# Optimization experiments

Hardware: AMD Instinct MI355X
Metric: run time of the kernel (lower is better)

Reference implementation:

```python
import jax, jax.numpy as jnp
import numpy as np

ATT_DIM = 512
HEADS = 8
HEAD_DIM = ATT_DIM // HEADS
D_IN = 512
LEFT_MASK = 256
RIGHT_MASK = 0
LARGE = 1e30


def pos_encoding(S, d):
    # Transformer-XL sinusoid table over relative positions S-1 .. -(S-1), length 2S-1.
    inv_freq = (1.0 / (10000.0 ** (np.arange(0, d, 2.0) / d))).astype(np.float32)
    pos = jnp.arange(S - 1, -S, -1, dtype=jnp.float32)          # [2S-1]
    ang = pos[:, None] * jnp.asarray(inv_freq)[None, :]          # [2S-1, d/2]
    # concat([sin, cos], -1) on a trailing singleton -> interleaved sin/cos per frequency
    return jnp.stack([jnp.sin(ang), jnp.cos(ang)], axis=-1).reshape(2 * S - 1, d)


def rel_shift(x):
    # x: [B, N, S, 2S-1] -> [B, N, S, S] with out[i, j] = x[i, S-1 - i + j]
    B, N, S, L = x.shape
    x = jnp.pad(x, ((0, 0), (0, 0), (0, 0), (1, 0)))             # [B,N,S,L+1]
    x = x.reshape(B, N, L + 1, S)[:, :, 1:, :]                   # [B,N,L,S]
    x = x.reshape(B, N, S, L)
    return x[:, :, :, :S]


def setup_inputs() -> dict:
    key = jax.random.key(0)
    ks = jax.random.split(key, 9)
    B, S, D = 2, 2048, D_IN
    scale = 0.02
    return {
        "x": jax.random.normal(ks[0], (B, S, D), dtype=jnp.float32),
        "Wq": jax.random.normal(ks[1], (D, ATT_DIM), dtype=jnp.float32) * scale,
        "b_con": jax.random.normal(ks[2], (ATT_DIM,), dtype=jnp.float32) * scale,
        "b_rel": jax.random.normal(ks[3], (ATT_DIM,), dtype=jnp.float32) * scale,
        "Wk": jax.random.normal(ks[4], (D, ATT_DIM), dtype=jnp.float32) * scale,
        "Wkr": jax.random.normal(ks[5], (D_IN, ATT_DIM), dtype=jnp.float32) * scale,
        "Wv": jax.random.normal(ks[6], (D, ATT_DIM), dtype=jnp.float32) * scale,
        "bv": jax.random.normal(ks[7], (ATT_DIM,), dtype=jnp.float32) * scale,
        "x_len": jax.random.randint(ks[8], (B,), 1, S + 1).astype(jnp.int32),
    }


def reference(x, Wq, b_con, b_rel, Wk, Wkr, Wv, bv, x_len):
    B, S, D = x.shape
    N, Dh = HEADS, HEAD_DIM

    # content/relative query share the kernel (TiedDense) with separate biases
    q_lin = jnp.einsum('bsd,de->bse', x, Wq)
    q_con = (q_lin + b_con).reshape(B, S, N, Dh)
    q_rel = (q_lin + b_rel).reshape(B, S, N, Dh)
    k_con = jnp.einsum('bsd,de->bse', x, Wk).reshape(B, S, N, Dh)

    content_energy = jnp.einsum('bind,bjnd->bnij', q_con, k_con)  # [B,N,S,S]

    pos_emb = pos_encoding(S, D_IN)                               # [2S-1, D]
    k_rel = (pos_emb @ Wkr).reshape(2 * S - 1, N, Dh)
    relative_energy = jnp.einsum('bind,jnd->bnij', q_rel, k_rel)  # [B,N,S,2S-1]
    relative_energy = rel_shift(relative_energy)                  # [B,N,S,S]

    energy = (content_energy + relative_energy) / jnp.sqrt(jnp.float32(Dh))

    # sequence mask over keys (broadcast [B,1,1,S]) * banded mask (band_part)
    j = jnp.arange(S)
    seq_mask = (j[None, :] < x_len[:, None]).astype(jnp.float32)[:, None, None, :]
    i = jnp.arange(S)[:, None]
    band = ((i - j[None, :] <= LEFT_MASK) & (j[None, :] - i <= RIGHT_MASK)).astype(jnp.float32)
    mask = seq_mask * band[None, None, :, :]

    masked_energy = energy - (1.0 - mask) * LARGE
    attention = jax.nn.softmax(masked_energy, axis=-1)

    v = (jnp.einsum('bsd,de->bse', x, Wv) + bv).reshape(B, S, N, Dh)
    context = jnp.einsum('bnij,bjnd->bind', attention, v).reshape(B, S, N * Dh)
    return context
```

## Files before the change

kernel.cpp:

```cpp
#include <hip/hip_runtime.h>
#include <math.h>

#define S_ 2048
#define NH 8
#define CSL 320
#define LP 72

typedef __attribute__((ext_vector_type(8))) short short8;
typedef __attribute__((ext_vector_type(4))) float f32x4;
typedef unsigned short ushort_t;

__device__ __forceinline__ short bf16r(float x) {
    union { float f; unsigned u; } v; v.f = x;
    unsigned r = v.u + 0x7fffu + ((v.u >> 16) & 1u);
    return (short)(r >> 16);
}
__device__ __forceinline__ float b2f(ushort_t h) {
    union { float f; unsigned u; } v; v.u = ((unsigned)h) << 16; return v.f;
}

__global__ __launch_bounds__(256) void prep_kernel(
    const float* __restrict__ x,
    const float* __restrict__ Wq, const float* __restrict__ Wk,
    const float* __restrict__ Wv, const float* __restrict__ Wkr,
    ushort_t* __restrict__ WTq, ushort_t* __restrict__ WTk,
    ushort_t* __restrict__ WTv, ushort_t* __restrict__ WTkr,
    ushort_t* __restrict__ pos, ushort_t* __restrict__ xb16)
{
    const int widx = blockIdx.z;
    const int t = threadIdx.x;
    if (widx == 4) {
        const int base = blockIdx.y * 8 + blockIdx.x;
        const float C = -0.051905126482615036f;
        const int f = t;
#pragma unroll
        for (int rep = 0; rep < 6; ++rep) {
            const int r = base + rep * 64;
            unsigned pk = 0;
            if (r <= 256) {
                float ang = (float)r * exp2f(C * (float)f);
                unsigned s = (unsigned)(ushort_t)bf16r(sinf(ang));
                unsigned c = (unsigned)(ushort_t)bf16r(cosf(ang));
                pk = s | (c << 16);
            }
            ((unsigned*)pos)[(size_t)r * 256 + f] = pk;
        }
        return;
    }
    if (widx == 5) {
        const int sub = blockIdx.y * 8 + blockIdx.x;
        const size_t base = (size_t)sub * 32768;
#pragma unroll
        for (int it = 0; it < 8; ++it) {
            const size_t idx = base + (size_t)it * 4096 + (size_t)t * 16;
            const float* src = &x[idx];
            ushort_t t16[16];
#pragma unroll
            for (int u = 0; u < 16; ++u) t16[u] = (ushort_t)bf16r(src[u]);
            *(short8*)&xb16[idx]     = *(short8*)&t16[0];
            *(short8*)&xb16[idx + 8] = *(short8*)&t16[8];
        }
        return;
    }
    const float* W = (widx == 0) ? Wq : (widx == 1) ? Wk : (widx == 2) ? Wv : Wkr;
    ushort_t* WT   = (widx == 0) ? WTq : (widx == 1) ? WTk : (widx == 2) ? WTv : WTkr;
    const int k0 = blockIdx.x * 64, n0 = blockIdx.y * 64;
    __shared__ __align__(16) ushort_t T[64][72];
    const int srow = t >> 2, sc0 = (t & 3) * 16;
    const float* src = &W[(size_t)(k0 + srow) * 512 + n0 + sc0];
#pragma unroll
    for (int u = 0; u < 16; ++u) T[sc0 + u][srow] = (ushort_t)bf16r(src[u]);
    __syncthreads();
    ushort_t* dst = &WT[(size_t)(n0 + srow) * 512 + k0 + sc0];
    *(short8*)dst       = *(const short8*)&T[srow][sc0];
    *(short8*)(dst + 8) = *(const short8*)&T[srow][sc0 + 8];
}

__global__ __launch_bounds__(256) void qkv_gemm(
    const ushort_t* __restrict__ xb16,
    const ushort_t* __restrict__ WTq, const ushort_t* __restrict__ WTk,
    const ushort_t* __restrict__ WTv,
    const ushort_t* __restrict__ pos, const ushort_t* __restrict__ WTkr,
    const float* __restrict__ b_con, const float* __restrict__ b_rel,
    const float* __restrict__ bv, const int* __restrict__ xlen_p,
    ushort_t* __restrict__ qcon, ushort_t* __restrict__ qrel,
    ushort_t* __restrict__ kout, ushort_t* __restrict__ vT,
    ushort_t* __restrict__ krel)
{
    const int widx = blockIdx.y >> 3;
    const int tid = threadIdx.x, lane = tid & 63, w = tid >> 6;
    const int quad = lane >> 4, l16 = lane & 15;

    __shared__ __align__(16) ushort_t A_lds[128][40];
    __shared__ __align__(16) ushort_t B_lds[64][40];

    f32x4 acc[2][4];
#pragma unroll
    for (int mt = 0; mt < 2; ++mt)
#pragma unroll
        for (int nt = 0; nt < 4; ++nt) acc[mt][nt] = (f32x4){0.f, 0.f, 0.f, 0.f};

    const int arow = tid >> 1, ak0 = (tid & 1) * 16;
    const int brow = tid >> 2, bk0 = (tid & 3) * 8;

    if (widx < 2) {
        const int m0 = blockIdx.x * 128;
        {
            const int xl = xlen_p[m0 >> 11];
            const int s0 = m0 & 2047;
            if (widx == 0) { if (s0 >= xl + 256) return; }
            else           { if (s0 >= xl + 63)  return; }
        }
        const int n0 = (blockIdx.y & 7) * 64;
        const ushort_t* WT = (widx == 0) ? WTq : WTk;
        const ushort_t* xrow = &xb16[(size_t)(m0 + arow) * 512 + ak0];
        const ushort_t* wrow = &WT[(size_t)(n0 + brow) * 512 + bk0];

        short8 pa0 = *(const short8*)xrow;
        short8 pa1 = *(const short8*)(xrow + 8);
        short8 pb  = *(const short8*)wrow;

#pragma unroll 1
        for (int k0 = 0; k0 < 512; k0 += 32) {
            __syncthreads();
            *(short8*)&A_lds[arow][ak0]     = pa0;
            *(short8*)&A_lds[arow][ak0 + 8] = pa1;
            *(short8*)&B_lds[brow][bk0]     = pb;
            if (k0 < 480) {
                pa0 = *(const short8*)(xrow + k0 + 32);
                pa1 = *(const short8*)(xrow + k0 + 40);
                pb  = *(const short8*)(wrow + k0 + 32);
            }
            __syncthreads();
            short8 a0 = *(const short8*)&A_lds[w * 32 + l16][quad * 8];
            short8 a1 = *(const short8*)&A_lds[w * 32 + 16 + l16][quad * 8];
#pragma unroll
            for (int nt = 0; nt < 4; ++nt) {
                short8 bb = *(const short8*)&B_lds[nt * 16 + l16][quad * 8];
                acc[0][nt] = __builtin_amdgcn_mfma_f32_16x16x32_bf16(a0, bb, acc[0][nt], 0, 0, 0);
                acc[1][nt] = __builtin_amdgcn_mfma_f32_16x16x32_bf16(a1, bb, acc[1][nt], 0, 0, 0);
            }
        }

#pragma unroll
        for (int nt = 0; nt < 4; ++nt) {
            const int col = n0 + nt * 16 + l16;
            float bc = 0.f, br = 0.f;
            if (widx == 0) { bc = b_con[col]; br = b_rel[col]; }
#pragma unroll
            for (int mt = 0; mt < 2; ++mt) {
#pragma unroll
                for (int reg = 0; reg < 4; ++reg) {
                    const size_t m = (size_t)(m0 + w * 32 + mt * 16 + quad * 4 + reg);
                    const float val = acc[mt][nt][reg];
                    if (widx == 0) {
                        qcon[m * 512 + col] = (ushort_t)bf16r((val + bc) * 0.125f);
                        qrel[m * 512 + col] = (ushort_t)bf16r((val + br) * 0.125f);
                    } else {
                        kout[m * 512 + col] = (ushort_t)bf16r(val);
                    }
                }
            }
        }
    } else if (widx == 2) {
        const int vb = (blockIdx.y & 7) * 32 + blockIdx.x;
        const int m0d = (vb & 3) * 128;
        const int n0j = (vb >> 2) * 64;
        const ushort_t* wrow = &WTv[(size_t)(m0d + arow) * 512 + ak0];
        const ushort_t* xrow = &xb16[(size_t)(n0j + brow) * 512 + bk0];

        short8 pa0 = *(const short8*)wrow;
        short8 pa1 = *(const short8*)(wrow + 8);
        short8 pb  = *(const short8*)xrow;

#pragma unroll 1
        for (int k0 = 0; k0 < 512; k0 += 32) {
            __syncthreads();
            *(short8*)&A_lds[arow][ak0]     = pa0;
            *(short8*)&A_lds[arow][ak0 + 8] = pa1;
            *(short8*)&B_lds[brow][bk0]     = pb;
            if (k0 < 480) {
                pa0 = *(const short8*)(wrow + k0 + 32);
                pa1 = *(const short8*)(wrow + k0 + 40);
                pb  = *(const short8*)(xrow + k0 + 32);
            }
            __syncthreads();
            short8 a0 = *(const short8*)&A_lds[w * 32 + l16][quad * 8];
            short8 a1 = *(const short8*)&A_lds[w * 32 + 16 + l16][quad * 8];
#pragma unroll
            for (int nt = 0; nt < 4; ++nt) {
                short8 bb = *(const short8*)&B_lds[nt * 16 + l16][quad * 8];
                acc[0][nt] = __builtin_amdgcn_mfma_f32_16x16x32_bf16(a0, bb, acc[0][nt], 0, 0, 0);
                acc[1][nt] = __builtin_amdgcn_mfma_f32_16x16x32_bf16(a1, bb, acc[1][nt], 0, 0, 0);
            }
        }

        const int b = n0j >> 11;
#pragma unroll
        for (int mt = 0; mt < 2; ++mt) {
#pragma unroll
            for (int reg = 0; reg < 4; ++reg) {
                const int d = m0d + w * 32 + mt * 16 + quad * 4 + reg;
                const int n = d >> 6, dd = d & 63;
                const float bvv = bv[d];
#pragma unroll
                for (int nt = 0; nt < 4; ++nt) {
                    const int s = (n0j + nt * 16 + l16) & 2047;
                    vT[((size_t)((b * NH + n) * 64 + dd)) * 2048 + s] =
                        (ushort_t)bf16r(acc[mt][nt][reg] + bvv);
                }
            }
        }
    } else {
        if (blockIdx.x >= 24) return;
        const int m0 = (blockIdx.x >> 3) * 128;
        const int n0 = (blockIdx.x & 7) * 64;
        const ushort_t* prow = &pos[(size_t)(m0 + arow) * 512 + ak0];
        const ushort_t* wrow = &WTkr[(size_t)(n0 + brow) * 512 + bk0];

        short8 pa0 = *(const short8*)prow;
        short8 pa1 = *(const short8*)(prow + 8);
        short8 pb  = *(const short8*)wrow;

#pragma unroll 1
        for (int k0 = 0; k0 < 512; k0 += 32) {
            __syncthreads();
            *(short8*)&A_lds[arow][ak0]     = pa0;
            *(short8*)&A_lds[arow][ak0 + 8] = pa1;
            *(short8*)&B_lds[brow][bk0]     = pb;
            if (k0 < 480) {
                pa0 = *(const short8*)(prow + k0 + 32);
                pa1 = *(const short8*)(prow + k0 + 40);
                pb  = *(const short8*)(wrow + k0 + 32);
            }
            __syncthreads();
            short8 a0 = *(const short8*)&A_lds[w * 32 + l16][quad * 8];
            short8 a1 = *(const short8*)&A_lds[w * 32 + 16 + l16][quad * 8];
#pragma unroll
            for (int nt = 0; nt < 4; ++nt) {
                short8 bb = *(const short8*)&B_lds[nt * 16 + l16][quad * 8];
                acc[0][nt] = __builtin_amdgcn_mfma_f32_16x16x32_bf16(a0, bb, acc[0][nt], 0, 0, 0);
                acc[1][nt] = __builtin_amdgcn_mfma_f32_16x16x32_bf16(a1, bb, acc[1][nt], 0, 0, 0);
            }
        }

#pragma unroll
        for (int nt = 0; nt < 4; ++nt) {
            const int col = n0 + nt * 16 + l16;
#pragma unroll
            for (int mt = 0; mt < 2; ++mt)
#pragma unroll
                for (int reg = 0; reg < 4; ++reg) {
                    const size_t m = (size_t)(m0 + w * 32 + mt * 16 + quad * 4 + reg);
                    krel[m * 512 + col] = (ushort_t)bf16r(acc[mt][nt][reg]);
                }
        }
    }
}

__global__ __launch_bounds__(256) void rel_gemm(
    const ushort_t* __restrict__ qrel, const ushort_t* __restrict__ krel,
    const ushort_t* __restrict__ vT, const int* __restrict__ xlen_p,
    ushort_t* __restrict__ R3, float* __restrict__ vmean)
{
    const int tile = blockIdx.x, n = blockIdx.y, b = blockIdx.z;
    const int tid = threadIdx.x, lane = tid & 63, w = tid >> 6;
    const int quad = lane >> 4, l16 = lane & 15;

    __shared__ __align__(16) ushort_t A_lds[128][LP];
    __shared__ __align__(16) ushort_t B_lds[64][LP];

    if (tile == 16) {
        const int row = tid >> 2, seg = tid & 3;
        const ushort_t* src = &vT[((size_t)((b * NH + n) * 64 + row)) * 2048 + seg * 512];
        float sum = 0.f;
        for (int it = 0; it < 64; ++it) {
            short8 h = *(const short8*)(src + it * 8);
#pragma unroll
            for (int u = 0; u < 8; ++u) sum += b2f((ushort_t)h[u]);
        }
        float* scratch = (float*)A_lds;
        scratch[row * 4 + seg] = sum;
        __syncthreads();
        if (tid < 64) {
            float s = scratch[tid * 4] + scratch[tid * 4 + 1]
                    + scratch[tid * 4 + 2] + scratch[tid * 4 + 3];
            vmean[(size_t)b * 512 + n * 64 + tid] = s * (1.0f / (float)S_);
        }
        return;
    }

    const int i0 = tile * 128;
    if (i0 >= xlen_p[b] + 256) return;

    {
        const int srow = tid >> 1, sc0 = (tid & 1) * 32;
        const ushort_t* src = &qrel[((size_t)b * S_ + i0 + srow) * 512 + n * 64 + sc0];
#pragma unroll
        for (int u = 0; u < 4; ++u)
            *(short8*)&A_lds[srow][sc0 + u * 8] = *(const short8*)(src + u * 8);
    }

    const size_t rbase3 = (size_t)(b * NH + n) * S_ * CSL;
    const int srow2 = tid >> 2, sc2 = (tid & 3) * 16;

    short8 pb0, pb1;
    auto issueB = [&](int rc) {
        const ushort_t* src = &krel[(size_t)(rc * 64 + srow2) * 512 + n * 64 + sc2];
        pb0 = *(const short8*)src;
        pb1 = *(const short8*)(src + 8);
    };
    issueB(0);

#pragma unroll 1
    for (int rc = 0; rc < 5; ++rc) {
        __syncthreads();
        *(short8*)&B_lds[srow2][sc2]     = pb0;
        *(short8*)&B_lds[srow2][sc2 + 8] = pb1;
        if (rc < 4) issueB(rc + 1);
        __syncthreads();

        short8 a[2][2];
#pragma unroll
        for (int mt = 0; mt < 2; ++mt) {
            a[mt][0] = *(const short8*)&A_lds[w * 32 + mt * 16 + l16][quad * 8];
            a[mt][1] = *(const short8*)&A_lds[w * 32 + mt * 16 + l16][quad * 8 + 32];
        }
#pragma unroll
        for (int nt = 0; nt < 4; ++nt) {
            short8 b0 = *(const short8*)&B_lds[nt * 16 + l16][quad * 8];
            short8 b1 = *(const short8*)&B_lds[nt * 16 + l16][quad * 8 + 32];
            const int r = rc * 64 + nt * 16 + l16;
#pragma unroll
            for (int mt = 0; mt < 2; ++mt) {
                f32x4 s = (f32x4){0.f, 0.f, 0.f, 0.f};
                s = __builtin_amdgcn_mfma_f32_16x16x32_bf16(a[mt][0], b0, s, 0, 0, 0);
                s = __builtin_amdgcn_mfma_f32_16x16x32_bf16(a[mt][1], b1, s, 0, 0, 0);
                if (r <= 256) {
#pragma unroll
                    for (int reg = 0; reg < 4; ++reg) {
                        const int ig = i0 + w * 32 + mt * 16 + quad * 4 + reg;
                        const int cslot = (ig & 63) + 256 - r;
                        R3[rbase3 + (size_t)ig * CSL + cslot] = (ushort_t)bf16r(s[reg]);
                    }
                }
            }
        }
    }
}

__global__ __launch_bounds__(256) void attn_kernel(
    const ushort_t* __restrict__ qcon, const ushort_t* __restrict__ kbuf,
    const ushort_t* __restrict__ vT, const ushort_t* __restrict__ R3,
    const float* __restrict__ vmean, const int* __restrict__ xlen_p,
    float* __restrict__ out)
{
    const int bx = blockIdx.x;
    const int tile = ((bx & 7) << 2) | (bx >> 3);
    const int n = blockIdx.y, b = blockIdx.z;
    const int i0 = tile * 64;
    const int tid = threadIdx.x, lane = tid & 63, w = tid >> 6;
    const int quad = lane >> 4, l16 = lane & 15;
    const int xlen = xlen_p[b];

    if (i0 >= xlen + 256) {
        const int row = tid >> 2, cf = (tid & 3) * 16;
        const float* vm = &vmean[(size_t)b * 512 + n * 64 + cf];
        float* dst = &out[((size_t)b * S_ + i0 + row) * 512 + n * 64 + cf];
#pragma unroll
        for (int u = 0; u < 16; u += 4)
            *(float4*)&dst[u] = *(const float4*)&vm[u];
        return;
    }
    int nchunk = (xlen - i0 + 256 + 63) >> 6;
    if (nchunk > 5) nchunk = 5;
    const int c0 = (i0 < 256) ? ((256 - i0) >> 6) : 0;

    __shared__ __align__(16) ushort_t k_lds[64][LP];
    __shared__ __align__(16) ushort_t vT_lds[64][LP];
    __shared__ __align__(16) ushort_t Rl_lds[64][LP];

    const ushort_t* qc = &qcon[((size_t)b * S_ + i0 + w * 16 + l16) * 512 + n * 64 + quad * 8];
    const short8 aq0 = *(const short8*)qc;
    const short8 aq1 = *(const short8*)(qc + 32);

    f32x4 Oa[4];
#pragma unroll
    for (int nt = 0; nt < 4; ++nt) Oa[nt] = (f32x4){0.f, 0.f, 0.f, 0.f};
    float lpart[4] = {};

    const size_t rbase3 = (size_t)(b * NH + n) * S_ * CSL;
    const size_t vTbase = (size_t)((b * NH + n) * 64) * 2048;
    const int srow = tid >> 2, sc0 = (tid & 3) * 16;

    short8 kr[2], vr[2], rr[2], kn[2], vn[2], rn[2];

    auto issue = [&](int c, short8* kd, short8* vd, short8* rd) {
        const int jc0 = i0 - 256 + c * 64;
        const ushort_t* ks = &kbuf[((size_t)b * S_ + jc0 + srow) * 512 + n * 64 + sc0];
        kd[0] = *(const short8*)ks;
        kd[1] = *(const short8*)(ks + 8);
        const ushort_t* vs = &vT[vTbase + (size_t)srow * 2048 + jc0 + sc0];
        vd[0] = *(const short8*)vs;
        vd[1] = *(const short8*)(vs + 8);
        const ushort_t* Rs = &R3[rbase3 + (size_t)(i0 + srow) * CSL + c * 64 + sc0];
        rd[0] = *(const short8*)Rs;
        rd[1] = *(const short8*)(Rs + 8);
    };

    issue(c0, kr, vr, rr);

#pragma unroll 1
    for (int c = c0; c < nchunk; ++c) {
        const int jc0 = i0 - 256 + c * 64;
        __syncthreads();
        *(short8*)&k_lds[srow][sc0]      = kr[0];
        *(short8*)&k_lds[srow][sc0 + 8]  = kr[1];
        *(short8*)&vT_lds[srow][sc0]     = vr[0];
        *(short8*)&vT_lds[srow][sc0 + 8] = vr[1];
        *(short8*)&Rl_lds[srow][sc0]     = rr[0];
        *(short8*)&Rl_lds[srow][sc0 + 8] = rr[1];
        if (c + 1 < nchunk) issue(c + 1, kn, vn, rn);
        __syncthreads();

        f32x4 Sacc[4];
#pragma unroll
        for (int jt = 0; jt < 4; ++jt) {
            short8 bk0 = *(const short8*)&k_lds[jt * 16 + l16][quad * 8];
            short8 bk1 = *(const short8*)&k_lds[jt * 16 + l16][quad * 8 + 32];
            f32x4 s = (f32x4){0.f, 0.f, 0.f, 0.f};
            s = __builtin_amdgcn_mfma_f32_16x16x32_bf16(aq0, bk0, s, 0, 0, 0);
            s = __builtin_amdgcn_mfma_f32_16x16x32_bf16(aq1, bk1, s, 0, 0, 0);
            Sacc[jt] = s;
        }

#pragma unroll
        for (int jt = 0; jt < 4; ++jt) {
#pragma unroll
            for (int reg = 0; reg < 4; ++reg) {
                const int row = w * 16 + quad * 4 + reg;
                const int i = i0 + row;
                const int j = jc0 + jt * 16 + l16;
                const int r = i - j;
                const bool valid = (j < xlen) && (r >= 0) && (r <= 256);
                float rvv = b2f(Rl_lds[row][jt * 16 + l16]);
                float e = valid ? __expf(Sacc[jt][reg] + rvv) : 0.f;
                lpart[reg] += e;
                Rl_lds[row][jt * 16 + l16] = (ushort_t)bf16r(e);
            }
        }

        short8 ap0 = *(const short8*)&Rl_lds[w * 16 + l16][quad * 8];
        short8 ap1 = *(const short8*)&Rl_lds[w * 16 + l16][quad * 8 + 32];
#pragma unroll
        for (int nt = 0; nt < 4; ++nt) {
            short8 bv0 = *(const short8*)&vT_lds[nt * 16 + l16][quad * 8];
            short8 bv1 = *(const short8*)&vT_lds[nt * 16 + l16][quad * 8 + 32];
            Oa[nt] = __builtin_amdgcn_mfma_f32_16x16x32_bf16(ap0, bv0, Oa[nt], 0, 0, 0);
            Oa[nt] = __builtin_amdgcn_mfma_f32_16x16x32_bf16(ap1, bv1, Oa[nt], 0, 0, 0);
        }

        kr[0] = kn[0]; kr[1] = kn[1];
        vr[0] = vn[0]; vr[1] = vn[1];
        rr[0] = rn[0]; rr[1] = rn[1];
    }

#pragma unroll
    for (int reg = 0; reg < 4; ++reg) {
#pragma unroll
        for (int off = 1; off < 16; off <<= 1)
            lpart[reg] += __shfl_xor(lpart[reg], off, 64);
    }

#pragma unroll
    for (int reg = 0; reg < 4; ++reg) {
        const int i = i0 + w * 16 + quad * 4 + reg;
        const bool dead = (i >= xlen + 256);
        const float linv = 1.0f / lpart[reg];
#pragma unroll
        for (int nt = 0; nt < 4; ++nt) {
            const int d = n * 64 + nt * 16 + l16;
            float val = dead ? vmean[(size_t)b * 512 + d] : Oa[nt][reg] * linv;
            out[((size_t)b * S_ + i) * 512 + d] = val;
        }
    }
}

extern "C" void kernel_launch(void* const* d_in, const int* in_sizes, int n_in,
                              void* d_out, int out_size, void* d_ws, size_t ws_size,
                              hipStream_t stream) {
    const float* x     = (const float*)d_in[0];
    const float* Wq    = (const float*)d_in[1];
    const float* b_con = (const float*)d_in[2];
    const float* b_rel = (const float*)d_in[3];
    const float* Wk    = (const float*)d_in[4];
    const float* Wkr   = (const float*)d_in[5];
    const float* Wv    = (const float*)d_in[6];
    const float* bv    = (const float*)d_in[7];
    const int*   xlen  = (const int*)d_in[8];
    float* out = (float*)d_out;

    float* ws = (float*)d_ws;
    float* vmean = ws;
    ushort_t* ub   = (ushort_t*)(vmean + 1024);
    ushort_t* R3   = ub;
    ushort_t* qcon = R3   + 10485760;
    ushort_t* kbuf = qcon + 2097152;
    ushort_t* vT   = kbuf + 2097152;
    ushort_t* qrel = vT   + 2097152;
    ushort_t* xb16 = qrel + 2097152;
    ushort_t* krel = xb16 + 2097152;
    ushort_t* pos  = krel + 196608;
    ushort_t* WTq  = pos  + 196608;
    ushort_t* WTk  = WTq + 262144;
    ushort_t* WTv  = WTk + 262144;
    ushort_t* WTkr = WTv + 262144;

    prep_kernel<<<dim3(8, 8, 6), 256, 0, stream>>>(x, Wq, Wk, Wv, Wkr,
                                                   WTq, WTk, WTv, WTkr, pos, xb16);
    qkv_gemm<<<dim3(32, 25), 256, 0, stream>>>(xb16, WTq, WTk, WTv, pos, WTkr,
                                               b_con, b_rel, bv, xlen,
                                               qcon, qrel, kbuf, vT, krel);
    rel_gemm<<<dim3(17, 8, 2), 256, 0, stream>>>(qrel, krel, vT, xlen, R3, vmean);
    attn_kernel<<<dim3(32, 8, 2), 256, 0, stream>>>(qcon, kbuf, vT, R3, vmean,
                                                    xlen, out);
}
```

Before: 127.4 us.

## Fuse rel-energy GEMM into Q projection and compute krel and vmean in prep

Drops the separate rel_gemm launch. The Q-projection blocks now keep q_rel in LDS and immediately compute the banded relative-energy tile into R3, so q_rel no longer goes through global memory. The k_rel projection moves into prep_kernel, which generates the sinusoid table on the fly and transposes Wkr inline, replacing the separate pos and WTkr buffers. vmean is now derived from mean(x) @ Wv + bv using column partial sums computed in prep, rather than by summing vT. This saves a launch and several global round trips, but makes the Q blocks longer and puts sin/cos evaluation on the krel GEMM path.

After: 152.1 us. 1.19x slower.

```diff
diff --git a/kernel.cpp b/kernel.cpp
--- a/kernel.cpp
+++ b/kernel.cpp
@@ -24,30 +24,17 @@
     const float* __restrict__ Wq, const float* __restrict__ Wk,
     const float* __restrict__ Wv, const float* __restrict__ Wkr,
     ushort_t* __restrict__ WTq, ushort_t* __restrict__ WTk,
-    ushort_t* __restrict__ WTv, ushort_t* __restrict__ WTkr,
-    ushort_t* __restrict__ pos, ushort_t* __restrict__ xb16)
+    ushort_t* __restrict__ WTv, ushort_t* __restrict__ xb16,
+    float* __restrict__ xpart, ushort_t* __restrict__ krel)
 {
     const int widx = blockIdx.z;
     const int t = threadIdx.x;
-    if (widx == 4) {
-        const int base = blockIdx.y * 8 + blockIdx.x;
-        const float C = -0.051905126482615036f;
-        const int f = t;
-#pragma unroll
-        for (int rep = 0; rep < 6; ++rep) {
-            const int r = base + rep * 64;
-            unsigned pk = 0;
-            if (r <= 256) {
-                float ang = (float)r * exp2f(C * (float)f);
-                unsigned s = (unsigned)(ushort_t)bf16r(sinf(ang));
-                unsigned c = (unsigned)(ushort_t)bf16r(cosf(ang));
-                pk = s | (c << 16);
-            }
-            ((unsigned*)pos)[(size_t)r * 256 + f] = pk;
-        }
-        return;
-    }
-    if (widx == 5) {
+
+    __shared__ __align__(16) ushort_t T[64][72];
+    __shared__ __align__(16) ushort_t Ak[128][40];
+    __shared__ __align__(16) ushort_t Bk[64][40];
+
+    if (widx == 3) {
         const int sub = blockIdx.y * 8 + blockIdx.x;
         const size_t base = (size_t)sub * 32768;
 #pragma unroll
@@ -62,10 +49,90 @@
         }
         return;
     }
-    const float* W = (widx == 0) ? Wq : (widx == 1) ? Wk : (widx == 2) ? Wv : Wkr;
-    ushort_t* WT   = (widx == 0) ? WTq : (widx == 1) ? WTk : (widx == 2) ? WTv : WTkr;
+    if (widx == 4) {
+        const int sub = blockIdx.y * 8 + blockIdx.x;
+        const int b = sub >> 5, rb = sub & 31;
+        const float* src = &x[((size_t)b * 2048 + (size_t)rb * 64) * 512];
+        float s0 = 0.f, s1 = 0.f;
+        for (int r = 0; r < 64; ++r) {
+            s0 += src[(size_t)r * 512 + t];
+            s1 += src[(size_t)r * 512 + t + 256];
+        }
+        xpart[(size_t)sub * 512 + t]       = s0;
+        xpart[(size_t)sub * 512 + t + 256] = s1;
+        return;
+    }
+    if (widx == 5) {
+        const int idx = blockIdx.y * 8 + blockIdx.x;
+        if (idx >= 24) return;
+        const int m0 = (idx >> 3) * 128;
+        const int n0 = (idx & 7) * 64;
+        const int lane = t & 63, w = t >> 6;
+        const int quad = lane >> 4, l16 = lane & 15;
+        const float C = -0.051905126482615036f;
+
+        f32x4 acc[2][4];
+#pragma unroll
+        for (int mt = 0; mt < 2; ++mt)
+#pragma unroll
+            for (int nt = 0; nt < 4; ++nt) acc[mt][nt] = (f32x4){0.f, 0.f, 0.f, 0.f};
+
+        const int arow = t >> 1, af0 = (t & 1) * 16;
+        const int bkr = t >> 3, bc0 = (t & 7) * 8;
+        const int r = m0 + arow;
+
+#pragma unroll 1
+        for (int k0 = 0; k0 < 512; k0 += 32) {
+            __syncthreads();
+            {
+                ushort_t a16[16];
+                if (r <= 256) {
+#pragma unroll
+                    for (int p = 0; p < 8; ++p) {
+                        const int k = k0 + af0 + 2 * p;
+                        const float ang = (float)r * exp2f(C * (float)(k >> 1));
+                        a16[2 * p]     = (ushort_t)bf16r(sinf(ang));
+                        a16[2 * p + 1] = (ushort_t)bf16r(cosf(ang));
+                    }
+                } else {
+#pragma unroll
+                    for (int u = 0; u < 16; ++u) a16[u] = 0;
+                }
+                *(short8*)&Ak[arow][af0]     = *(short8*)&a16[0];
+                *(short8*)&Ak[arow][af0 + 8] = *(short8*)&a16[8];
+            }
+            {
+                const float* wsrc = &Wkr[(size_t)(k0 + bkr) * 512 + n0 + bc0];
+#pragma unroll
+                for (int u = 0; u < 8; ++u)
+                    Bk[bc0 + u][bkr] = (ushort_t)bf16r(wsrc[u]);
+            }
+            __syncthreads();
+            short8 a0 = *(const short8*)&Ak[w * 32 + l16][quad * 8];
+            short8 a1 = *(const short8*)&Ak[w * 32 + 16 + l16][quad * 8];
+#pragma unroll
+            for (int nt = 0; nt < 4; ++nt) {
+                short8 bb = *(const short8*)&Bk[nt * 16 + l16][quad * 8];
+                acc[0][nt] = __builtin_amdgcn_mfma_f32_16x16x32_bf16(a0, bb, acc[0][nt], 0, 0, 0);
+                acc[1][nt] = __builtin_amdgcn_mfma_f32_16x16x32_bf16(a1, bb, acc[1][nt], 0, 0, 0);
+            }
+        }
+#pragma unroll
+        for (int nt = 0; nt < 4; ++nt) {
+            const int col = n0 + nt * 16 + l16;
+#pragma unroll
+            for (int mt = 0; mt < 2; ++mt)
+#pragma unroll
+                for (int reg = 0; reg < 4; ++reg) {
+                    const size_t m = (size_t)(m0 + w * 32 + mt * 16 + quad * 4 + reg);
+                    krel[m * 512 + col] = (ushort_t)bf16r(acc[mt][nt][reg]);
+                }
+        }
+        return;
+    }
+    const float* W = (widx == 0) ? Wq : (widx == 1) ? Wk : Wv;
+    ushort_t* WT   = (widx == 0) ? WTq : (widx == 1) ? WTk : WTv;
     const int k0 = blockIdx.x * 64, n0 = blockIdx.y * 64;
-    __shared__ __align__(16) ushort_t T[64][72];
     const int srow = t >> 2, sc0 = (t & 3) * 16;
     const float* src = &W[(size_t)(k0 + srow) * 512 + n0 + sc0];
 #pragma unroll
@@ -79,20 +146,23 @@
 __global__ __launch_bounds__(256) void qkv_gemm(
     const ushort_t* __restrict__ xb16,
     const ushort_t* __restrict__ WTq, const ushort_t* __restrict__ WTk,
-    const ushort_t* __restrict__ WTv,
-    const ushort_t* __restrict__ pos, const ushort_t* __restrict__ WTkr,
+    const ushort_t* __restrict__ WTv, const ushort_t* __restrict__ krel,
     const float* __restrict__ b_con, const float* __restrict__ b_rel,
     const float* __restrict__ bv, const int* __restrict__ xlen_p,
-    ushort_t* __restrict__ qcon, ushort_t* __restrict__ qrel,
-    ushort_t* __restrict__ kout, ushort_t* __restrict__ vT,
-    ushort_t* __restrict__ krel)
+    const float* __restrict__ xpart,
+    ushort_t* __restrict__ qcon, ushort_t* __restrict__ kout,
+    ushort_t* __restrict__ vT, ushort_t* __restrict__ R3,
+    float* __restrict__ vmean)
 {
     const int widx = blockIdx.y >> 3;
     const int tid = threadIdx.x, lane = tid & 63, w = tid >> 6;
     const int quad = lane >> 4, l16 = lane & 15;
 
-    __shared__ __align__(16) ushort_t A_lds[128][40];
-    __shared__ __align__(16) ushort_t B_lds[64][40];
+    __shared__ __align__(16) ushort_t arena[13824];
+#define AQ(r, c) arena[(r) * 40 + (c)]
+#define BQ(r, c) arena[5120 + (r) * 40 + (c)]
+#define QL(r, c) arena[(r) * 72 + (c)]
+#define BR(r, c) arena[9216 + (r) * 72 + (c)]
 
     f32x4 acc[2][4];
 #pragma unroll
@@ -105,12 +175,10 @@
 
     if (widx < 2) {
         const int m0 = blockIdx.x * 128;
-        {
-            const int xl = xlen_p[m0 >> 11];
-            const int s0 = m0 & 2047;
-            if (widx == 0) { if (s0 >= xl + 256) return; }
-            else           { if (s0 >= xl + 63)  return; }
-        }
+        const int xl = xlen_p[m0 >> 11];
+        const int s0 = m0 & 2047;
+        if (widx == 0) { if (s0 >= xl + 256) return; }
+        else           { if (s0 >= xl + 63)  return; }
         const int n0 = (blockIdx.y & 7) * 64;
         const ushort_t* WT = (widx == 0) ? WTq : WTk;
         const ushort_t* xrow = &xb16[(size_t)(m0 + arow) * 512 + ak0];
@@ -123,41 +191,101 @@
 #pragma unroll 1
         for (int k0 = 0; k0 < 512; k0 += 32) {
             __syncthreads();
-            *(short8*)&A_lds[arow][ak0]     = pa0;
-            *(short8*)&A_lds[arow][ak0 + 8] = pa1;
-            *(short8*)&B_lds[brow][bk0]     = pb;
+            *(short8*)&AQ(arow, ak0)     = pa0;
+            *(short8*)&AQ(arow, ak0 + 8) = pa1;
+            *(short8*)&BQ(brow, bk0)     = pb;
             if (k0 < 480) {
                 pa0 = *(const short8*)(xrow + k0 + 32);
                 pa1 = *(const short8*)(xrow + k0 + 40);
                 pb  = *(const short8*)(wrow + k0 + 32);
             }
             __syncthreads();
-            short8 a0 = *(const short8*)&A_lds[w * 32 + l16][quad * 8];
-            short8 a1 = *(const short8*)&A_lds[w * 32 + 16 + l16][quad * 8];
+            short8 a0 = *(const short8*)&AQ(w * 32 + l16, quad * 8);
+            short8 a1 = *(const short8*)&AQ(w * 32 + 16 + l16, quad * 8);
 #pragma unroll
             for (int nt = 0; nt < 4; ++nt) {
-                short8 bb = *(const short8*)&B_lds[nt * 16 + l16][quad * 8];
+                short8 bb = *(const short8*)&BQ(nt * 16 + l16, quad * 8);
                 acc[0][nt] = __builtin_amdgcn_mfma_f32_16x16x32_bf16(a0, bb, acc[0][nt], 0, 0, 0);
                 acc[1][nt] = __builtin_amdgcn_mfma_f32_16x16x32_bf16(a1, bb, acc[1][nt], 0, 0, 0);
             }
         }
 
+        if (widx == 1) {
+#pragma unroll
+            for (int nt = 0; nt < 4; ++nt) {
+                const int col = n0 + nt * 16 + l16;
+#pragma unroll
+                for (int mt = 0; mt < 2; ++mt)
+#pragma unroll
+                    for (int reg = 0; reg < 4; ++reg) {
+                        const size_t m = (size_t)(m0 + w * 32 + mt * 16 + quad * 4 + reg);
+                        kout[m * 512 + col] = (ushort_t)bf16r(acc[mt][nt][reg]);
+                    }
+            }
+            return;
+        }
+
+        __syncthreads();
 #pragma unroll
         for (int nt = 0; nt < 4; ++nt) {
             const int col = n0 + nt * 16 + l16;
-            float bc = 0.f, br = 0.f;
-            if (widx == 0) { bc = b_con[col]; br = b_rel[col]; }
+            const float bc = b_con[col], br = b_rel[col];
 #pragma unroll
             for (int mt = 0; mt < 2; ++mt) {
 #pragma unroll
                 for (int reg = 0; reg < 4; ++reg) {
-                    const size_t m = (size_t)(m0 + w * 32 + mt * 16 + quad * 4 + reg);
+                    const int rloc = w * 32 + mt * 16 + quad * 4 + reg;
+                    const size_t m = (size_t)(m0 + rloc);
                     const float val = acc[mt][nt][reg];
-                    if (widx == 0) {
-                        qcon[m * 512 + col] = (ushort_t)bf16r((val + bc) * 0.125f);
-                        qrel[m * 512 + col] = (ushort_t)bf16r((val + br) * 0.125f);
-                    } else {
-                        kout[m * 512 + col] = (ushort_t)bf16r(val);
+                    qcon[m * 512 + col] = (ushort_t)bf16r((val + bc) * 0.125f);
+                    QL(rloc, nt * 16 + l16) = (ushort_t)bf16r((val + br) * 0.125f);
+                }
+            }
+        }
+
+        const int b = m0 >> 11, n = n0 >> 6, iloc0 = m0 & 2047;
+        const size_t rbase3 = (size_t)(b * NH + n) * S_ * CSL;
+        const int srow2 = tid >> 2, sc2 = (tid & 3) * 16;
+
+        short8 pb0, pb1;
+        auto issueB = [&](int rc) {
+            const ushort_t* src = &krel[(size_t)(rc * 64 + srow2) * 512 + n0 + sc2];
+            pb0 = *(const short8*)src;
+            pb1 = *(const short8*)(src + 8);
+        };
+        issueB(0);
+
+#pragma unroll 1
+        for (int rc = 0; rc < 5; ++rc) {
+            __syncthreads();
+            *(short8*)&BR(srow2, sc2)     = pb0;
+            *(short8*)&BR(srow2, sc2 + 8) = pb1;
+            if (rc < 4) issueB(rc + 1);
+            __syncthreads();
+
+            short8 a[2][2];
+#pragma unroll
+            for (int mt = 0; mt < 2; ++mt) {
+                a[mt][0] = *(const short8*)&QL(w * 32 + mt * 16 + l16, quad * 8);
+                a[mt][1] = *(const short8*)&QL(w * 32 + mt * 16 + l16, quad * 8 + 32);
+            }
+#pragma unroll
+            for (int nt = 0; nt < 4; ++nt) {
+                short8 b0 = *(const short8*)&BR(nt * 16 + l16, quad * 8);
+                short8 b1 = *(const short8*)&BR(nt * 16 + l16, quad * 8 + 32);
+                const int r = rc * 64 + nt * 16 + l16;
+#pragma unroll
+                for (int mt = 0; mt < 2; ++mt) {
+                    f32x4 s = (f32x4){0.f, 0.f, 0.f, 0.f};
+                    s = __builtin_amdgcn_mfma_f32_16x16x32_bf16(a[mt][0], b0, s, 0, 0, 0);
+                    s = __builtin_amdgcn_mfma_f32_16x16x32_bf16(a[mt][1], b1, s, 0, 0, 0);
+                    if (r <= 256) {
+#pragma unroll
+                        for (int reg = 0; reg < 4; ++reg) {
+                            const int ig = iloc0 + w * 32 + mt * 16 + quad * 4 + reg;
+                            const int cslot = (ig & 63) + 256 - r;
+                            R3[rbase3 + (size_t)ig * CSL + cslot] = (ushort_t)bf16r(s[reg]);
+                        }
                     }
                 }
             }
@@ -176,20 +304,20 @@
 #pragma unroll 1
         for (int k0 = 0; k0 < 512; k0 += 32) {
             __syncthreads();
-            *(short8*)&A_lds[arow][ak0]     = pa0;
-            *(short8*)&A_lds[arow][ak0 + 8] = pa1;
-            *(short8*)&B_lds[brow][bk0]     = pb;
+            *(short8*)&AQ(arow, ak0)     = pa0;
+            *(short8*)&AQ(arow, ak0 + 8) = pa1;
+            *(short8*)&BQ(brow, bk0)     = pb;
             if (k0 < 480) {
                 pa0 = *(const short8*)(wrow + k0 + 32);
                 pa1 = *(const short8*)(wrow + k0 + 40);
                 pb  = *(const short8*)(xrow + k0 + 32);
             }
             __syncthreads();
-            short8 a0 = *(const short8*)&A_lds[w * 32 + l16][quad * 8];
-            short8 a1 = *(const short8*)&A_lds[w * 32 + 16 + l16][quad * 8];
+            short8 a0 = *(const short8*)&AQ(w * 32 + l16, quad * 8);
+            short8 a1 = *(const short8*)&AQ(w * 32 + 16 + l16, quad * 8);
 #pragma unroll
             for (int nt = 0; nt < 4; ++nt) {
-                short8 bb = *(const short8*)&B_lds[nt * 16 + l16][quad * 8];
+                short8 bb = *(const short8*)&BQ(nt * 16 + l16, quad * 8);
                 acc[0][nt] = __builtin_amdgcn_mfma_f32_16x16x32_bf16(a0, bb, acc[0][nt], 0, 0, 0);
                 acc[1][nt] = __builtin_amdgcn_mfma_f32_16x16x32_bf16(a1, bb, acc[1][nt], 0, 0, 0);
             }
@@ -212,141 +340,38 @@
             }
         }
     } else {
-        if (blockIdx.x >= 24) return;
-        const int m0 = (blockIdx.x >> 3) * 128;
-        const int n0 = (blockIdx.x & 7) * 64;
-        const ushort_t* prow = &pos[(size_t)(m0 + arow) * 512 + ak0];
-        const ushort_t* wrow = &WTkr[(size_t)(n0 + brow) * 512 + bk0];
-
-        short8 pa0 = *(const short8*)prow;
-        short8 pa1 = *(const short8*)(prow + 8);
-        short8 pb  = *(const short8*)wrow;
-
-#pragma unroll 1
-        for (int k0 = 0; k0 < 512; k0 += 32) {
-            __syncthreads();
-            *(short8*)&A_lds[arow][ak0]     = pa0;
-            *(short8*)&A_lds[arow][ak0 + 8] = pa1;
-            *(short8*)&B_lds[brow][bk0]     = pb;
-            if (k0 < 480) {
-                pa0 = *(const short8*)(prow + k0 + 32);
-                pa1 = *(const short8*)(prow + k0 + 40);
-                pb  = *(const short8*)(wrow + k0 + 32);
-            }
-            __syncthreads();
-            short8 a0 = *(const short8*)&A_lds[w * 32 + l16][quad * 8];
-            short8 a1 = *(const short8*)&A_lds[w * 32 + 16 + l16][quad * 8];
-#pragma unroll
-            for (int nt = 0; nt < 4; ++nt) {
-                short8 bb = *(const short8*)&B_lds[nt * 16 + l16][quad * 8];
-                acc[0][nt] = __builtin_amdgcn_mfma_f32_16x16x32_bf16(a0, bb, acc[0][nt], 0, 0, 0);
-                acc[1][nt] = __builtin_amdgcn_mfma_f32_16x16x32_bf16(a1, bb, acc[1][nt], 0, 0, 0);
-            }
-        }
-
-#pragma unroll
-        for (int nt = 0; nt < 4; ++nt) {
-            const int col = n0 + nt * 16 + l16;
-#pragma unroll
-            for (int mt = 0; mt < 2; ++mt)
-#pragma unroll
-                for (int reg = 0; reg < 4; ++reg) {
-                    const size_t m = (size_t)(m0 + w * 32 + mt * 16 + quad * 4 + reg);
-                    krel[m * 512 + col] = (ushort_t)bf16r(acc[mt][nt][reg]);
-                }
-        }
-    }
-}
-
-__global__ __launch_bounds__(256) void rel_gemm(
-    const ushort_t* __restrict__ qrel, const ushort_t* __restrict__ krel,
-    const ushort_t* __restrict__ vT, const int* __restrict__ xlen_p,
-    ushort_t* __restrict__ R3, float* __restrict__ vmean)
-{
-    const int tile = blockIdx.x, n = blockIdx.y, b = blockIdx.z;
-    const int tid = threadIdx.x, lane = tid & 63, w = tid >> 6;
-    const int quad = lane >> 4, l16 = lane & 15;
-
-    __shared__ __align__(16) ushort_t A_lds[128][LP];
-    __shared__ __align__(16) ushort_t B_lds[64][LP];
-
-    if (tile == 16) {
-        const int row = tid >> 2, seg = tid & 3;
-        const ushort_t* src = &vT[((size_t)((b * NH + n) * 64 + row)) * 2048 + seg * 512];
-        float sum = 0.f;
-        for (int it = 0; it < 64; ++it) {
-            short8 h = *(const short8*)(src + it * 8);
-#pragma unroll
-            for (int u = 0; u < 8; ++u) sum += b2f((ushort_t)h[u]);
-        }
-        float* scratch = (float*)A_lds;
-        scratch[row * 4 + seg] = sum;
+        if (blockIdx.x >= 8) return;
+        float* xm = (float*)arena;
+        for (int idx = tid; idx < 1024; idx += 256) {
+            const int bb = idx >> 9, k = idx & 511;
+            float s = 0.f;
+            for (int p = 0; p < 32; ++p)
+                s += xpart[(size_t)(bb * 32 + p) * 512 + k];
+            xm[bb * 512 + k] = s * (1.0f / 2048.0f);
+        }
         __syncthreads();
         if (tid < 64) {
-            float s = scratch[tid * 4] + scratch[tid * 4 + 1]
-                    + scratch[tid * 4 + 2] + scratch[tid * 4 + 3];
-            vmean[(size_t)b * 512 + n * 64 + tid] = s * (1.0f / (float)S_);
-        }
-        return;
-    }
-
-    const int i0 = tile * 128;
-    if (i0 >= xlen_p[b] + 256) return;
-
-    {
-        const int srow = tid >> 1, sc0 = (tid & 1) * 32;
-        const ushort_t* src = &qrel[((size_t)b * S_ + i0 + srow) * 512 + n * 64 + sc0];
-#pragma unroll
-        for (int u = 0; u < 4; ++u)
-            *(short8*)&A_lds[srow][sc0 + u * 8] = *(const short8*)(src + u * 8);
-    }
-
-    const size_t rbase3 = (size_t)(b * NH + n) * S_ * CSL;
-    const int srow2 = tid >> 2, sc2 = (tid & 3) * 16;
-
-    short8 pb0, pb1;
-    auto issueB = [&](int rc) {
-        const ushort_t* src = &krel[(size_t)(rc * 64 + srow2) * 512 + n * 64 + sc2];
-        pb0 = *(const short8*)src;
-        pb1 = *(const short8*)(src + 8);
-    };
-    issueB(0);
-
-#pragma unroll 1
-    for (int rc = 0; rc < 5; ++rc) {
-        __syncthreads();
-        *(short8*)&B_lds[srow2][sc2]     = pb0;
-        *(short8*)&B_lds[srow2][sc2 + 8] = pb1;
-        if (rc < 4) issueB(rc + 1);
-        __syncthreads();
-
-        short8 a[2][2];
-#pragma unroll
-        for (int mt = 0; mt < 2; ++mt) {
-            a[mt][0] = *(const short8*)&A_lds[w * 32 + mt * 16 + l16][quad * 8];
-            a[mt][1] = *(const short8*)&A_lds[w * 32 + mt * 16 + l16][quad * 8 + 32];
-        }
-#pragma unroll
-        for (int nt = 0; nt < 4; ++nt) {
-            short8 b0 = *(const short8*)&B_lds[nt * 16 + l16][quad * 8];
-            short8 b1 = *(const short8*)&B_lds[nt * 16 + l16][quad * 8 + 32];
-            const int r = rc * 64 + nt * 16 + l16;
-#pragma unroll
-            for (int mt = 0; mt < 2; ++mt) {
-                f32x4 s = (f32x4){0.f, 0.f, 0.f, 0.f};
-                s = __builtin_amdgcn_mfma_f32_16x16x32_bf16(a[mt][0], b0, s, 0, 0, 0);
-                s = __builtin_amdgcn_mfma_f32_16x16x32_bf16(a[mt][1], b1, s, 0, 0, 0);
-                if (r <= 256) {
-#pragma unroll
-                    for (int reg = 0; reg < 4; ++reg) {
-                        const int ig = i0 + w * 32 + mt * 16 + quad * 4 + reg;
-                        const int cslot = (ig & 63) + 256 - r;
-                        R3[rbase3 + (size_t)ig * CSL + cslot] = (ushort_t)bf16r(s[reg]);
-                    }
+            const int d = blockIdx.x * 64 + tid;
+            const ushort_t* wrow = &WTv[(size_t)d * 512];
+            float a0 = 0.f, a1 = 0.f;
+            for (int k = 0; k < 512; k += 8) {
+                short8 wv = *(const short8*)(wrow + k);
+#pragma unroll
+                for (int u = 0; u < 8; ++u) {
+                    const float wf = b2f((ushort_t)wv[u]);
+                    a0 += xm[k + u] * wf;
+                    a1 += xm[512 + k + u] * wf;
                 }
             }
-        }
-    }
+            const float bvd = bv[d];
+            vmean[d]       = a0 + bvd;
+            vmean[512 + d] = a1 + bvd;
+        }
+    }
+#undef AQ
+#undef BQ
+#undef QL
+#undef BR
 }
 
 __global__ __launch_bounds__(256) void attn_kernel(
@@ -502,26 +527,24 @@
 
     float* ws = (float*)d_ws;
     float* vmean = ws;
-    ushort_t* ub   = (ushort_t*)(vmean + 1024);
+    float* xpart = vmean + 1024;
+    ushort_t* ub   = (ushort_t*)(xpart + 32768);
     ushort_t* R3   = ub;
     ushort_t* qcon = R3   + 10485760;
     ushort_t* kbuf = qcon + 2097152;
     ushort_t* vT   = kbuf + 2097152;
-    ushort_t* qrel = vT   + 2097152;
-    ushort_t* xb16 = qrel + 2097152;
+    ushort_t* xb16 = vT   + 2097152;
     ushort_t* krel = xb16 + 2097152;
-    ushort_t* pos  = krel + 196608;
-    ushort_t* WTq  = pos  + 196608;
+    ushort_t* WTq  = krel + 196608;
     ushort_t* WTk  = WTq + 262144;
     ushort_t* WTv  = WTk + 262144;
-    ushort_t* WTkr = WTv + 262144;
 
     prep_kernel<<<dim3(8, 8, 6), 256, 0, stream>>>(x, Wq, Wk, Wv, Wkr,
-                                                   WTq, WTk, WTv, WTkr, pos, xb16);
-    qkv_gemm<<<dim3(32, 25), 256, 0, stream>>>(xb16, WTq, WTk, WTv, pos, WTkr,
-                                               b_con, b_rel, bv, xlen,
-                                               qcon, qrel, kbuf, vT, krel);
-    rel_gemm<<<dim3(17, 8, 2), 256, 0, stream>>>(qrel, krel, vT, xlen, R3, vmean);
+                                                   WTq, WTk, WTv, xb16,
+                                                   xpart, krel);
+    qkv_gemm<<<dim3(32, 25), 256, 0, stream>>>(xb16, WTq, WTk, WTv, krel,
+                                               b_con, b_rel, bv, xlen, xpart,
+                                               qcon, kbuf, vT, R3, vmean);
     attn_kernel<<<dim3(32, 8, 2), 256, 0, stream>>>(qcon, kbuf, vT, R3, vmean,
                                                     xlen, out);
 }
```

## Widen Q/K GEMM tiles to 128x128 and halve rel_gemm row tiles

Applied to the files above, without the earlier changes.

The Q/K projection blocks now compute 128x128 output tiles instead of 128x64, halving the number of Q/K blocks and reusing each loaded x tile across twice as many columns. The grid shrinks from 25 to 17 rows. Separately, rel_gemm now processes 64 query rows per block instead of 128, doubling its block count to raise parallelism. The trade-off is higher accumulator register pressure in qkv_gemm, and more krel reloads across the extra rel_gemm blocks.

Result: slower. 133.5 us (+4.8%).

```diff
diff --git a/kernel.cpp b/kernel.cpp
--- a/kernel.cpp
+++ b/kernel.cpp
@@ -87,23 +87,17 @@
     ushort_t* __restrict__ kout, ushort_t* __restrict__ vT,
     ushort_t* __restrict__ krel)
 {
-    const int widx = blockIdx.y >> 3;
+    const int by = blockIdx.y;
     const int tid = threadIdx.x, lane = tid & 63, w = tid >> 6;
     const int quad = lane >> 4, l16 = lane & 15;
 
     __shared__ __align__(16) ushort_t A_lds[128][40];
-    __shared__ __align__(16) ushort_t B_lds[64][40];
-
-    f32x4 acc[2][4];
-#pragma unroll
-    for (int mt = 0; mt < 2; ++mt)
-#pragma unroll
-        for (int nt = 0; nt < 4; ++nt) acc[mt][nt] = (f32x4){0.f, 0.f, 0.f, 0.f};
+    __shared__ __align__(16) ushort_t B_lds[128][40];
 
     const int arow = tid >> 1, ak0 = (tid & 1) * 16;
-    const int brow = tid >> 2, bk0 = (tid & 3) * 8;
-
-    if (widx < 2) {
+
+    if (by < 8) {
+        const int widx = by >> 2;
         const int m0 = blockIdx.x * 128;
         {
             const int xl = xlen_p[m0 >> 11];
@@ -111,31 +105,40 @@
             if (widx == 0) { if (s0 >= xl + 256) return; }
             else           { if (s0 >= xl + 63)  return; }
         }
-        const int n0 = (blockIdx.y & 7) * 64;
+        const int n0 = (by & 3) * 128;
         const ushort_t* WT = (widx == 0) ? WTq : WTk;
         const ushort_t* xrow = &xb16[(size_t)(m0 + arow) * 512 + ak0];
-        const ushort_t* wrow = &WT[(size_t)(n0 + brow) * 512 + bk0];
+        const ushort_t* wrow = &WT[(size_t)(n0 + arow) * 512 + ak0];
+
+        f32x4 acc[2][8];
+#pragma unroll
+        for (int mt = 0; mt < 2; ++mt)
+#pragma unroll
+            for (int nt = 0; nt < 8; ++nt) acc[mt][nt] = (f32x4){0.f, 0.f, 0.f, 0.f};
 
         short8 pa0 = *(const short8*)xrow;
         short8 pa1 = *(const short8*)(xrow + 8);
-        short8 pb  = *(const short8*)wrow;
+        short8 pb0 = *(const short8*)wrow;
+        short8 pb1 = *(const short8*)(wrow + 8);
 
 #pragma unroll 1
         for (int k0 = 0; k0 < 512; k0 += 32) {
             __syncthreads();
             *(short8*)&A_lds[arow][ak0]     = pa0;
             *(short8*)&A_lds[arow][ak0 + 8] = pa1;
-            *(short8*)&B_lds[brow][bk0]     = pb;
+            *(short8*)&B_lds[arow][ak0]     = pb0;
+            *(short8*)&B_lds[arow][ak0 + 8] = pb1;
             if (k0 < 480) {
                 pa0 = *(const short8*)(xrow + k0 + 32);
                 pa1 = *(const short8*)(xrow + k0 + 40);
-                pb  = *(const short8*)(wrow + k0 + 32);
+                pb0 = *(const short8*)(wrow + k0 + 32);
+                pb1 = *(const short8*)(wrow + k0 + 40);
             }
             __syncthreads();
             short8 a0 = *(const short8*)&A_lds[w * 32 + l16][quad * 8];
             short8 a1 = *(const short8*)&A_lds[w * 32 + 16 + l16][quad * 8];
 #pragma unroll
-            for (int nt = 0; nt < 4; ++nt) {
+            for (int nt = 0; nt < 8; ++nt) {
                 short8 bb = *(const short8*)&B_lds[nt * 16 + l16][quad * 8];
                 acc[0][nt] = __builtin_amdgcn_mfma_f32_16x16x32_bf16(a0, bb, acc[0][nt], 0, 0, 0);
                 acc[1][nt] = __builtin_amdgcn_mfma_f32_16x16x32_bf16(a1, bb, acc[1][nt], 0, 0, 0);
@@ -143,7 +146,7 @@
         }
 
 #pragma unroll
-        for (int nt = 0; nt < 4; ++nt) {
+        for (int nt = 0; nt < 8; ++nt) {
             const int col = n0 + nt * 16 + l16;
             float bc = 0.f, br = 0.f;
             if (widx == 0) { bc = b_con[col]; br = b_rel[col]; }
@@ -162,12 +165,19 @@
                 }
             }
         }
-    } else if (widx == 2) {
-        const int vb = (blockIdx.y & 7) * 32 + blockIdx.x;
+    } else if (by < 16) {
+        const int brow = tid >> 2, bk0 = (tid & 3) * 8;
+        const int vb = (by & 7) * 32 + blockIdx.x;
         const int m0d = (vb & 3) * 128;
         const int n0j = (vb >> 2) * 64;
         const ushort_t* wrow = &WTv[(size_t)(m0d + arow) * 512 + ak0];
         const ushort_t* xrow = &xb16[(size_t)(n0j + brow) * 512 + bk0];
+
+        f32x4 acc[2][4];
+#pragma unroll
+        for (int mt = 0; mt < 2; ++mt)
+#pragma unroll
+            for (int nt = 0; nt < 4; ++nt) acc[mt][nt] = (f32x4){0.f, 0.f, 0.f, 0.f};
 
         short8 pa0 = *(const short8*)wrow;
         short8 pa1 = *(const short8*)(wrow + 8);
@@ -213,10 +223,17 @@
         }
     } else {
         if (blockIdx.x >= 24) return;
+        const int brow = tid >> 2, bk0 = (tid & 3) * 8;
         const int m0 = (blockIdx.x >> 3) * 128;
         const int n0 = (blockIdx.x & 7) * 64;
         const ushort_t* prow = &pos[(size_t)(m0 + arow) * 512 + ak0];
         const ushort_t* wrow = &WTkr[(size_t)(n0 + brow) * 512 + bk0];
+
+        f32x4 acc[2][4];
+#pragma unroll
+        for (int mt = 0; mt < 2; ++mt)
+#pragma unroll
+            for (int nt = 0; nt < 4; ++nt) acc[mt][nt] = (f32x4){0.f, 0.f, 0.f, 0.f};
 
         short8 pa0 = *(const short8*)prow;
         short8 pa1 = *(const short8*)(prow + 8);
@@ -267,10 +284,10 @@
     const int tid = threadIdx.x, lane = tid & 63, w = tid >> 6;
     const int quad = lane >> 4, l16 = lane & 15;
 
-    __shared__ __align__(16) ushort_t A_lds[128][LP];
+    __shared__ __align__(16) ushort_t A_lds[64][LP];
     __shared__ __align__(16) ushort_t B_lds[64][LP];
 
-    if (tile == 16) {
+    if (tile == 32) {
         const int row = tid >> 2, seg = tid & 3;
         const ushort_t* src = &vT[((size_t)((b * NH + n) * 64 + row)) * 2048 + seg * 512];
         float sum = 0.f;
@@ -290,15 +307,14 @@
         return;
     }
 
-    const int i0 = tile * 128;
+    const int i0 = tile * 64;
     if (i0 >= xlen_p[b] + 256) return;
 
     {
-        const int srow = tid >> 1, sc0 = (tid & 1) * 32;
+        const int srow = tid >> 2, sc0 = (tid & 3) * 16;
         const ushort_t* src = &qrel[((size_t)b * S_ + i0 + srow) * 512 + n * 64 + sc0];
-#pragma unroll
-        for (int u = 0; u < 4; ++u)
-            *(short8*)&A_lds[srow][sc0 + u * 8] = *(const short8*)(src + u * 8);
+        *(short8*)&A_lds[srow][sc0]     = *(const short8*)src;
+        *(short8*)&A_lds[srow][sc0 + 8] = *(const short8*)(src + 8);
     }
 
     const size_t rbase3 = (size_t)(b * NH + n) * S_ * CSL;
@@ -320,29 +336,22 @@
         if (rc < 4) issueB(rc + 1);
         __syncthreads();
 
-        short8 a[2][2];
-#pragma unroll
-        for (int mt = 0; mt < 2; ++mt) {
-            a[mt][0] = *(const short8*)&A_lds[w * 32 + mt * 16 + l16][quad * 8];
-            a[mt][1] = *(const short8*)&A_lds[w * 32 + mt * 16 + l16][quad * 8 + 32];
-        }
+        short8 a0 = *(const short8*)&A_lds[w * 16 + l16][quad * 8];
+        short8 a1 = *(const short8*)&A_lds[w * 16 + l16][quad * 8 + 32];
 #pragma unroll
         for (int nt = 0; nt < 4; ++nt) {
             short8 b0 = *(const short8*)&B_lds[nt * 16 + l16][quad * 8];
             short8 b1 = *(const short8*)&B_lds[nt * 16 + l16][quad * 8 + 32];
             const int r = rc * 64 + nt * 16 + l16;
-#pragma unroll
-            for (int mt = 0; mt < 2; ++mt) {
-                f32x4 s = (f32x4){0.f, 0.f, 0.f, 0.f};
-                s = __builtin_amdgcn_mfma_f32_16x16x32_bf16(a[mt][0], b0, s, 0, 0, 0);
-                s = __builtin_amdgcn_mfma_f32_16x16x32_bf16(a[mt][1], b1, s, 0, 0, 0);
-                if (r <= 256) {
-#pragma unroll
-                    for (int reg = 0; reg < 4; ++reg) {
-                        const int ig = i0 + w * 32 + mt * 16 + quad * 4 + reg;
-                        const int cslot = (ig & 63) + 256 - r;
-                        R3[rbase3 + (size_t)ig * CSL + cslot] = (ushort_t)bf16r(s[reg]);
-                    }
+            f32x4 s = (f32x4){0.f, 0.f, 0.f, 0.f};
+            s = __builtin_amdgcn_mfma_f32_16x16x32_bf16(a0, b0, s, 0, 0, 0);
+            s = __builtin_amdgcn_mfma_f32_16x16x32_bf16(a1, b1, s, 0, 0, 0);
+            if (r <= 256) {
+#pragma unroll
+                for (int reg = 0; reg < 4; ++reg) {
+                    const int ig = i0 + w * 16 + quad * 4 + reg;
+                    const int cslot = (ig & 63) + 256 - r;
+                    R3[rbase3 + (size_t)ig * CSL + cslot] = (ushort_t)bf16r(s[reg]);
                 }
             }
         }
@@ -518,10 +527,10 @@
 
     prep_kernel<<<dim3(8, 8, 6), 256, 0, stream>>>(x, Wq, Wk, Wv, Wkr,
                                                    WTq, WTk, WTv, WTkr, pos, xb16);
-    qkv_gemm<<<dim3(32, 25), 256, 0, stream>>>(xb16, WTq, WTk, WTv, pos, WTkr,
+    qkv_gemm<<<dim3(32, 17), 256, 0, stream>>>(xb16, WTq, WTk, WTv, pos, WTkr,
                                                b_con, b_rel, bv, xlen,
                                                qcon, qrel, kbuf, vT, krel);
-    rel_gemm<<<dim3(17, 8, 2), 256, 0, stream>>>(qrel, krel, vT, xlen, R3, vmean);
+    rel_gemm<<<dim3(33, 8, 2), 256, 0, stream>>>(qrel, krel, vT, xlen, R3, vmean);
     attn_kernel<<<dim3(32, 8, 2), 256, 0, stream>>>(qcon, kbuf, vT, R3, vmean,
                                                     xlen, out);
 }
```
